# Kernel optimization log

Hardware: AMD Instinct MI355X
Metric: run time of the kernel (lower is better)

Reference implementation:

```python
import jax, jax.numpy as jnp
import numpy as np
from jax import lax
from jax.scipy.special import logsumexp

INSIZE = 256
NBASE = 4
SIZE = 2 * NBASE * (NBASE + 1)  # 40


def setup_inputs() -> dict:
    key = jax.random.key(0)
    kx, kw, kb = jax.random.split(key, 3)
    x = jax.random.normal(kx, (2048, 256, INSIZE), dtype=jnp.float32)
    W = jax.random.normal(kw, (SIZE, INSIZE), dtype=jnp.float32) / np.sqrt(INSIZE)
    b = 0.5 * jax.random.normal(kb, (SIZE,), dtype=jnp.float32)
    return {"x": x, "W": W, "b": b}


def global_norm_flipflop(scores):
    # scores: (T, N, C) with C = 2*nbase*(nbase+1)
    T, N, C = scores.shape
    nbase = int(np.sqrt(C / 2))
    assert 2 * nbase * (nbase + 1) == C

    fwd0 = jnp.zeros((N, 2 * nbase), dtype=scores.dtype)
    logZ0 = logsumexp(fwd0, axis=1, keepdims=True)  # (N, 1) = log(2*nbase)
    fwd0 = fwd0 - logZ0

    def step(carry, sc_t):
        fwd, logZ = carry
        # (N, nbase+1, 2*nbase): transition scores into each destination row
        sc = fwd[:, None, :] + sc_t.reshape(N, nbase + 1, 2 * nbase)
        base1 = logsumexp(sc[:, :nbase], axis=2)  # flip states (N, nbase)
        base2 = jnp.logaddexp(sc[:, nbase, :nbase], sc[:, nbase, nbase:])  # flop (N, nbase)
        new_state = jnp.concatenate([base1, base2], axis=1)  # (N, 2*nbase)
        factors = logsumexp(new_state, axis=1, keepdims=True)
        return (new_state - factors, logZ + factors), None

    (_, logZ), _ = lax.scan(step, (fwd0, logZ0), scores)
    return scores - logZ / T  # broadcast (N,1) over (T,N,C)


def reference(x, W, b):
    y = 5.0 * jnp.tanh(x @ W.T + b)  # (T, N, 40)
    return global_norm_flipflop(y)
```

## Files before the change

### kernel.cpp

```cpp
#include <hip/hip_runtime.h>
#include <hip/hip_bf16.h>

#define T_DIM 2048
#define N_DIM 256
#define K_DIM 256
#define C_DIM 40
#define CHUNK 32
#define NCHUNK 64
#define NTILES (T_DIM * N_DIM / 16)

#define LOG2E_F 1.44269504088896340736f
#define LN2_F   0.69314718055994530942f
#define NEGBIG  (-1.0e30f)

typedef short bf16x8 __attribute__((ext_vector_type(8)));
typedef float f32x4  __attribute__((ext_vector_type(4)));

__device__ __forceinline__ float fexp2(float x) { return exp2f(x); }
__device__ __forceinline__ float flog2(float x) { return log2f(x); }
__device__ __forceinline__ float frcp(float x) { return __frcp_rn(x); }

__device__ __forceinline__ unsigned int pk2(float a, float b)
{
    __hip_bfloat162 h = __float22bfloat162_rn(make_float2(a, b));
    unsigned int r;
    __builtin_memcpy(&r, &h, sizeof(r));
    return r;
}

__device__ __forceinline__ uint4 pack8u(float4 lo, float4 hi)
{
    uint4 t;
    t.x = pk2(lo.x, lo.y);
    t.y = pk2(lo.z, lo.w);
    t.z = pk2(hi.x, hi.y);
    t.w = pk2(hi.z, hi.w);
    return t;
}

__device__ __forceinline__ bf16x8 as_bf16x8(uint4 u)
{
    bf16x8 r;
    __builtin_memcpy(&r, &u, sizeof(r));
    return r;
}

__device__ __forceinline__ float tanh5(float v)
{
    const float e = fexp2(fabsf(v) * (2.0f * LOG2E_F));
    const float t = 1.0f - 2.0f * frcp(e + 1.0f);
    return 5.0f * copysignf(t, v);
}

__global__ __launch_bounds__(256, 4) void k1_gemm_tanh(
    const float* __restrict__ x, const float* __restrict__ W,
    const float* __restrict__ b, float* __restrict__ y)
{
    __shared__ __align__(16) uint4 wlds[24 * 64];
    __shared__ float blds[48];

    const int tid = threadIdx.x;

#pragma unroll
    for (int p = 0; p < 6; ++p) {
        const int f    = p * 256 + tid;
        const int l    = f & 63;
        const int frag = f >> 6;
        const int nt   = frag % 3;
        const int ks   = frag / 3;
        const int col  = nt * 16 + (l & 15);
        const int kg   = l >> 4;
        float4 lo = make_float4(0, 0, 0, 0), hi = lo;
        if (col < C_DIM) {
            lo = *(const float4*)(W + (size_t)col * K_DIM + ks * 32 + kg * 4);
            hi = *(const float4*)(W + (size_t)col * K_DIM + ks * 32 + 16 + kg * 4);
        }
        wlds[frag * 64 + l] = pack8u(lo, hi);
    }
    if (tid < 48) blds[tid] = (tid < C_DIM) ? b[tid] : 0.0f;
    __syncthreads();

    const int wave = tid >> 6;
    const int lane = tid & 63;
    const int lr   = lane & 15;
    const int kg   = lane >> 4;

    const float bc0 = blds[lr];
    const float bc1 = blds[16 + lr];
    const float bc2 = blds[32 + lr];

    const int wid = blockIdx.x * 4 + wave;

#pragma unroll 1
    for (int tile = wid; tile < NTILES; tile += 4096) {
        const float4* __restrict__ xp4 =
            (const float4*)(x + ((size_t)tile * 16 + lr) * K_DIM) + kg;

        f32x4 af0 = {bc0, bc0, bc0, bc0};
        f32x4 af1 = {bc1, bc1, bc1, bc1};
        f32x4 af2 = {bc2, bc2, bc2, bc2};

#pragma unroll
        for (int ks = 0; ks < 8; ++ks) {
            const float4 lo = xp4[ks * 8];
            const float4 hi = xp4[ks * 8 + 4];
            const bf16x8 a = as_bf16x8(pack8u(lo, hi));
            const bf16x8 w0 = *(const bf16x8*)&wlds[(ks * 3 + 0) * 64 + lane];
            const bf16x8 w1 = *(const bf16x8*)&wlds[(ks * 3 + 1) * 64 + lane];
            const bf16x8 w2 = *(const bf16x8*)&wlds[(ks * 3 + 2) * 64 + lane];
            af0 = __builtin_amdgcn_mfma_f32_16x16x32_bf16(a, w0, af0, 0, 0, 0);
            af1 = __builtin_amdgcn_mfma_f32_16x16x32_bf16(a, w1, af1, 0, 0, 0);
            af2 = __builtin_amdgcn_mfma_f32_16x16x32_bf16(a, w2, af2, 0, 0, 0);
        }

        float* __restrict__ yrow = y + ((size_t)tile * 16 + kg * 4) * C_DIM;
#pragma unroll
        for (int r = 0; r < 4; ++r) {
            yrow[r * C_DIM + lr]      = tanh5(af0[r]);
            yrow[r * C_DIM + 16 + lr] = tanh5(af1[r]);
            if (lr < 8)
                yrow[r * C_DIM + 32 + lr] = tanh5(af2[r]);
        }
    }
}

__global__ __launch_bounds__(256) void k2_chunks(
    const float* __restrict__ y, float* __restrict__ cmat)
{
    const int tid  = threadIdx.x;
    const int wave = tid >> 6;
    const int lane = tid & 63;
    const int task = lane >> 3;
    const int c    = lane & 7;
    const int g    = blockIdx.x & (NCHUNK - 1);
    const int n    = ((blockIdx.x >> 6) << 5) + (wave << 3) + task;

    float col[8];
#pragma unroll
    for (int j = 0; j < 8; ++j) col[j] = (j == c) ? 0.0f : NEGBIG;

    const float* __restrict__ yp =
        y + ((size_t)(g * CHUNK) * N_DIM + (size_t)n) * C_DIM;

#pragma unroll 1
    for (int s = 0; s < CHUNK; ++s) {
        float sc[C_DIM];
        const float4* p4 = (const float4*)yp;
#pragma unroll
        for (int q = 0; q < 10; ++q) {
            const float4 v = p4[q];
            sc[4 * q + 0] = v.x * LOG2E_F;
            sc[4 * q + 1] = v.y * LOG2E_F;
            sc[4 * q + 2] = v.z * LOG2E_F;
            sc[4 * q + 3] = v.w * LOG2E_F;
        }
        float nc[8];
#pragma unroll
        for (int d = 0; d < 4; ++d) {
            float tv[8];
#pragma unroll
            for (int j = 0; j < 8; ++j) tv[j] = sc[d * 8 + j] + col[j];
            float m = tv[0];
#pragma unroll
            for (int j = 1; j < 8; ++j) m = fmaxf(m, tv[j]);
            float ss = 0.0f;
#pragma unroll
            for (int j = 0; j < 8; ++j) ss += fexp2(tv[j] - m);
            nc[d] = m + flog2(ss);
        }
#pragma unroll
        for (int i = 0; i < 4; ++i) {
            const float a  = sc[32 + i] + col[i];
            const float bb = sc[36 + i] + col[i + 4];
            const float m  = fmaxf(a, bb);
            const float ss = fexp2(a - m) + fexp2(bb - m);
            nc[4 + i] = m + flog2(ss);
        }
#pragma unroll
        for (int j = 0; j < 8; ++j) col[j] = nc[j];
        yp += (size_t)N_DIM * C_DIM;
    }
    float* __restrict__ op = cmat + (((size_t)g * 8 + c) * N_DIM + n) * 8;
#pragma unroll
    for (int j = 0; j < 8; ++j) op[j] = col[j];
}

__global__ __launch_bounds__(256) void k3_combine(
    const float* __restrict__ cmat, float* __restrict__ corr)
{
    const int tid = threadIdx.x;
    const int d   = tid & 7;
    const int n   = blockIdx.x * 32 + (tid >> 3);

    float v[8];
#pragma unroll
    for (int j = 0; j < 8; ++j) v[j] = 0.0f;

#pragma unroll 1
    for (int g = 0; g < NCHUNK; ++g) {
        const float* mg = cmat + ((size_t)g * 8 * N_DIM + n) * 8 + d;
        float mm[8];
#pragma unroll
        for (int j = 0; j < 8; ++j) mm[j] = mg[(size_t)j * N_DIM * 8];
        float tv[8];
#pragma unroll
        for (int j = 0; j < 8; ++j) tv[j] = mm[j] + v[j];
        float m = tv[0];
#pragma unroll
        for (int j = 1; j < 8; ++j) m = fmaxf(m, tv[j]);
        float ss = 0.0f;
#pragma unroll
        for (int j = 0; j < 8; ++j) ss += fexp2(tv[j] - m);
        const float nv = m + flog2(ss);
#pragma unroll
        for (int j = 0; j < 8; ++j) v[j] = __shfl(nv, j, 8);
    }
    float m = v[0];
#pragma unroll
    for (int j = 1; j < 8; ++j) m = fmaxf(m, v[j]);
    float ss = 0.0f;
#pragma unroll
    for (int j = 0; j < 8; ++j) ss += fexp2(v[j] - m);
    const float lz2 = m + flog2(ss);
    if (d == 0) corr[n] = lz2 * LN2_F / (float)T_DIM;
}

__global__ __launch_bounds__(256) void k4_final(
    float* __restrict__ out, const float* __restrict__ corr)
{
    const unsigned int i = blockIdx.x * 256u + threadIdx.x;
    float4* o4 = (float4*)out;
    float4 v = o4[i];
    const unsigned int n = (i / 10u) & (N_DIM - 1);
    const float cr = corr[n];
    v.x -= cr; v.y -= cr; v.z -= cr; v.w -= cr;
    o4[i] = v;
}

extern "C" void kernel_launch(void* const* d_in, const int* in_sizes, int n_in,
                              void* d_out, int out_size, void* d_ws, size_t ws_size,
                              hipStream_t stream)
{
    const float* x = (const float*)d_in[0];
    const float* W = (const float*)d_in[1];
    const float* b = (const float*)d_in[2];
    float* y = (float*)d_out;

    float* cmat = (float*)d_ws;
    float* corr = (float*)d_ws + (size_t)NCHUNK * 8 * N_DIM * 8;

    hipLaunchKernelGGL(k1_gemm_tanh, dim3(1024), dim3(256), 0, stream, x, W, b, y);
    hipLaunchKernelGGL(k2_chunks,    dim3(512),  dim3(256), 0, stream, y, cmat);
    hipLaunchKernelGGL(k3_combine,   dim3(8),    dim3(256), 0, stream, cmat, corr);
    hipLaunchKernelGGL(k4_final,     dim3((T_DIM * N_DIM * C_DIM / 4) / 256),
                       dim3(256), 0, stream, y, corr);
}
```

Measured before the change: 264.6 us.

## Store tanh scores as bf16 intermediate and stage x through swizzled LDS with split-K waves

The GEMM kernel now loads 64-row x tiles cooperatively into XOR-swizzled shared memory as bf16. Two wave groups split K and reduce through LDS, with W fragments held in registers. The scores are written to a bf16 workspace instead of fp32 output. The recurrence and final kernels read bf16, and the final kernel writes fp32 output, which lowers intermediate traffic. This trades accuracy, since the output values are rounded to bf16, and adds block-level syncs per tile.

```diff
diff --git a/kernel.cpp b/kernel.cpp
--- a/kernel.cpp
+++ b/kernel.cpp
@@ -7,7 +7,7 @@
 #define C_DIM 40
 #define CHUNK 32
 #define NCHUNK 64
-#define NTILES (T_DIM * N_DIM / 16)
+#define NSUPER (T_DIM * N_DIM / 64)
 
 #define LOG2E_F 1.44269504088896340736f
 #define LN2_F   0.69314718055994530942f
@@ -45,6 +45,14 @@
     return r;
 }
 
+__device__ __forceinline__ unsigned short bf16r(float v)
+{
+    return (unsigned short)(pk2(v, 0.0f) & 0xffffu);
+}
+
+__device__ __forceinline__ float bl(unsigned int w) { return __uint_as_float(w << 16); }
+__device__ __forceinline__ float bh(unsigned int w) { return __uint_as_float(w & 0xffff0000u); }
+
 __device__ __forceinline__ float tanh5(float v)
 {
     const float e = fexp2(fabsf(v) * (2.0f * LOG2E_F));
@@ -52,80 +60,108 @@
     return 5.0f * copysignf(t, v);
 }
 
-__global__ __launch_bounds__(256, 4) void k1_gemm_tanh(
+__global__ __launch_bounds__(512, 4) void k1_gemm_tanh(
     const float* __restrict__ x, const float* __restrict__ W,
-    const float* __restrict__ b, float* __restrict__ y)
-{
-    __shared__ __align__(16) uint4 wlds[24 * 64];
-    __shared__ float blds[48];
-
-    const int tid = threadIdx.x;
-
-#pragma unroll
-    for (int p = 0; p < 6; ++p) {
-        const int f    = p * 256 + tid;
-        const int l    = f & 63;
-        const int frag = f >> 6;
-        const int nt   = frag % 3;
-        const int ks   = frag / 3;
-        const int col  = nt * 16 + (l & 15);
-        const int kg   = l >> 4;
-        float4 lo = make_float4(0, 0, 0, 0), hi = lo;
-        if (col < C_DIM) {
-            lo = *(const float4*)(W + (size_t)col * K_DIM + ks * 32 + kg * 4);
-            hi = *(const float4*)(W + (size_t)col * K_DIM + ks * 32 + 16 + kg * 4);
-        }
-        wlds[frag * 64 + l] = pack8u(lo, hi);
-    }
-    if (tid < 48) blds[tid] = (tid < C_DIM) ? b[tid] : 0.0f;
-    __syncthreads();
-
+    const float* __restrict__ b, unsigned short* __restrict__ yb)
+{
+    __shared__ __align__(16) unsigned char xl[64 * 512];
+    __shared__ __align__(16) float pl[4 * 12 * 64];
+
+    const int tid  = threadIdx.x;
     const int wave = tid >> 6;
     const int lane = tid & 63;
     const int lr   = lane & 15;
     const int kg   = lane >> 4;
-
-    const float bc0 = blds[lr];
-    const float bc1 = blds[16 + lr];
-    const float bc2 = blds[32 + lr];
-
-    const int wid = blockIdx.x * 4 + wave;
+    const int mt   = wave & 3;
+    const int kh   = wave >> 2;
+
+    const float bc0 = b[lr];
+    const float bc1 = b[16 + lr];
+    const float bc2 = (lr < 8) ? b[32 + lr] : 0.0f;
+
+    bf16x8 wf[4][3];
+#pragma unroll
+    for (int i = 0; i < 4; ++i) {
+        const int ks = kh * 4 + i;
+#pragma unroll
+        for (int nt = 0; nt < 3; ++nt) {
+            const int col = nt * 16 + lr;
+            float4 lo = make_float4(0, 0, 0, 0), hi = lo;
+            if (col < C_DIM) {
+                const float* wp = W + (size_t)col * K_DIM + ks * 32 + kg * 8;
+                lo = *(const float4*)wp;
+                hi = *(const float4*)(wp + 4);
+            }
+            wf[i][nt] = as_bf16x8(pack8u(lo, hi));
+        }
+    }
 
 #pragma unroll 1
-    for (int tile = wid; tile < NTILES; tile += 4096) {
-        const float4* __restrict__ xp4 =
-            (const float4*)(x + ((size_t)tile * 16 + lr) * K_DIM) + kg;
-
-        f32x4 af0 = {bc0, bc0, bc0, bc0};
-        f32x4 af1 = {bc1, bc1, bc1, bc1};
-        f32x4 af2 = {bc2, bc2, bc2, bc2};
-
-#pragma unroll
-        for (int ks = 0; ks < 8; ++ks) {
-            const float4 lo = xp4[ks * 8];
-            const float4 hi = xp4[ks * 8 + 4];
-            const bf16x8 a = as_bf16x8(pack8u(lo, hi));
-            const bf16x8 w0 = *(const bf16x8*)&wlds[(ks * 3 + 0) * 64 + lane];
-            const bf16x8 w1 = *(const bf16x8*)&wlds[(ks * 3 + 1) * 64 + lane];
-            const bf16x8 w2 = *(const bf16x8*)&wlds[(ks * 3 + 2) * 64 + lane];
-            af0 = __builtin_amdgcn_mfma_f32_16x16x32_bf16(a, w0, af0, 0, 0, 0);
-            af1 = __builtin_amdgcn_mfma_f32_16x16x32_bf16(a, w1, af1, 0, 0, 0);
-            af2 = __builtin_amdgcn_mfma_f32_16x16x32_bf16(a, w2, af2, 0, 0, 0);
-        }
-
-        float* __restrict__ yrow = y + ((size_t)tile * 16 + kg * 4) * C_DIM;
-#pragma unroll
-        for (int r = 0; r < 4; ++r) {
-            yrow[r * C_DIM + lr]      = tanh5(af0[r]);
-            yrow[r * C_DIM + 16 + lr] = tanh5(af1[r]);
-            if (lr < 8)
-                yrow[r * C_DIM + 32 + lr] = tanh5(af2[r]);
+    for (int st = blockIdx.x; st < NSUPER; st += gridDim.x) {
+        const float4* __restrict__ xg4 =
+            (const float4*)(x + (size_t)st * 64 * K_DIM);
+#pragma unroll
+        for (int p = 0; p < 8; ++p) {
+            const int f4  = p * 512 + tid;
+            const int row = f4 >> 6;
+            const int kq  = f4 & 63;
+            const float4 v = xg4[f4];
+            uint2 w2;
+            w2.x = pk2(v.x, v.y);
+            w2.y = pk2(v.z, v.w);
+            const int off = (row * 512 + kq * 8) ^ ((row & 7) << 4);
+            *(uint2*)(xl + off) = w2;
+        }
+        __syncthreads();
+
+        f32x4 af0, af1, af2;
+        if (kh == 0) {
+            af0 = (f32x4){bc0, bc0, bc0, bc0};
+            af1 = (f32x4){bc1, bc1, bc1, bc1};
+            af2 = (f32x4){bc2, bc2, bc2, bc2};
+        } else {
+            af0 = (f32x4){0.f, 0.f, 0.f, 0.f}; af1 = af0; af2 = af0;
+        }
+        const int rbase = (mt * 16 + lr) * 512;
+        const int swz   = (lr & 7) << 4;
+#pragma unroll
+        for (int i = 0; i < 4; ++i) {
+            const int ks = kh * 4 + i;
+            const bf16x8 a =
+                *(const bf16x8*)(xl + ((rbase + ks * 64 + kg * 16) ^ swz));
+            af0 = __builtin_amdgcn_mfma_f32_16x16x32_bf16(a, wf[i][0], af0, 0, 0, 0);
+            af1 = __builtin_amdgcn_mfma_f32_16x16x32_bf16(a, wf[i][1], af1, 0, 0, 0);
+            af2 = __builtin_amdgcn_mfma_f32_16x16x32_bf16(a, wf[i][2], af2, 0, 0, 0);
+        }
+
+        if (kh == 1) {
+            float* p = pl + (mt * 12) * 64 + lane;
+#pragma unroll
+            for (int j = 0; j < 4; ++j) p[j * 64]       = af0[j];
+#pragma unroll
+            for (int j = 0; j < 4; ++j) p[(4 + j) * 64] = af1[j];
+#pragma unroll
+            for (int j = 0; j < 4; ++j) p[(8 + j) * 64] = af2[j];
+        }
+        __syncthreads();
+
+        if (kh == 0) {
+            const float* p = pl + (mt * 12) * 64 + lane;
+            unsigned short* yr =
+                yb + ((size_t)st * 64 + mt * 16 + kg * 4) * C_DIM;
+#pragma unroll
+            for (int r = 0; r < 4; ++r) {
+                yr[r * C_DIM + lr]      = bf16r(tanh5(af0[r] + p[r * 64]));
+                yr[r * C_DIM + 16 + lr] = bf16r(tanh5(af1[r] + p[(4 + r) * 64]));
+                if (lr < 8)
+                    yr[r * C_DIM + 32 + lr] = bf16r(tanh5(af2[r] + p[(8 + r) * 64]));
+            }
         }
     }
 }
 
 __global__ __launch_bounds__(256) void k2_chunks(
-    const float* __restrict__ y, float* __restrict__ cmat)
+    const unsigned short* __restrict__ yb, float* __restrict__ cmat)
 {
     const int tid  = threadIdx.x;
     const int wave = tid >> 6;
@@ -139,20 +175,24 @@
 #pragma unroll
     for (int j = 0; j < 8; ++j) col[j] = (j == c) ? 0.0f : NEGBIG;
 
-    const float* __restrict__ yp =
-        y + ((size_t)(g * CHUNK) * N_DIM + (size_t)n) * C_DIM;
+    const unsigned short* __restrict__ yp =
+        yb + ((size_t)(g * CHUNK) * N_DIM + (size_t)n) * C_DIM;
 
 #pragma unroll 1
     for (int s = 0; s < CHUNK; ++s) {
         float sc[C_DIM];
-        const float4* p4 = (const float4*)yp;
-#pragma unroll
-        for (int q = 0; q < 10; ++q) {
-            const float4 v = p4[q];
-            sc[4 * q + 0] = v.x * LOG2E_F;
-            sc[4 * q + 1] = v.y * LOG2E_F;
-            sc[4 * q + 2] = v.z * LOG2E_F;
-            sc[4 * q + 3] = v.w * LOG2E_F;
+        const uint4* p4 = (const uint4*)yp;
+#pragma unroll
+        for (int q = 0; q < 5; ++q) {
+            const uint4 u = p4[q];
+            sc[8 * q + 0] = bl(u.x) * LOG2E_F;
+            sc[8 * q + 1] = bh(u.x) * LOG2E_F;
+            sc[8 * q + 2] = bl(u.y) * LOG2E_F;
+            sc[8 * q + 3] = bh(u.y) * LOG2E_F;
+            sc[8 * q + 4] = bl(u.z) * LOG2E_F;
+            sc[8 * q + 5] = bh(u.z) * LOG2E_F;
+            sc[8 * q + 6] = bl(u.w) * LOG2E_F;
+            sc[8 * q + 7] = bh(u.w) * LOG2E_F;
         }
         float nc[8];
 #pragma unroll
@@ -226,15 +266,20 @@
 }
 
 __global__ __launch_bounds__(256) void k4_final(
-    float* __restrict__ out, const float* __restrict__ corr)
-{
-    const unsigned int i = blockIdx.x * 256u + threadIdx.x;
+    const unsigned short* __restrict__ yb, const float* __restrict__ corr,
+    float* __restrict__ out)
+{
+    const int i = blockIdx.x * 256 + threadIdx.x;
+    const uint4 u = ((const uint4*)yb)[i];
+    const float cr = corr[(i / 5) & (N_DIM - 1)];
+    float4 o0, o1;
+    o0.x = bl(u.x) - cr; o0.y = bh(u.x) - cr;
+    o0.z = bl(u.y) - cr; o0.w = bh(u.y) - cr;
+    o1.x = bl(u.z) - cr; o1.y = bh(u.z) - cr;
+    o1.z = bl(u.w) - cr; o1.w = bh(u.w) - cr;
     float4* o4 = (float4*)out;
-    float4 v = o4[i];
-    const unsigned int n = (i / 10u) & (N_DIM - 1);
-    const float cr = corr[n];
-    v.x -= cr; v.y -= cr; v.z -= cr; v.w -= cr;
-    o4[i] = v;
+    o4[i * 2]     = o0;
+    o4[i * 2 + 1] = o1;
 }
 
 extern "C" void kernel_launch(void* const* d_in, const int* in_sizes, int n_in,
@@ -244,14 +289,15 @@
     const float* x = (const float*)d_in[0];
     const float* W = (const float*)d_in[1];
     const float* b = (const float*)d_in[2];
-    float* y = (float*)d_out;
-
-    float* cmat = (float*)d_ws;
-    float* corr = (float*)d_ws + (size_t)NCHUNK * 8 * N_DIM * 8;
-
-    hipLaunchKernelGGL(k1_gemm_tanh, dim3(1024), dim3(256), 0, stream, x, W, b, y);
-    hipLaunchKernelGGL(k2_chunks,    dim3(512),  dim3(256), 0, stream, y, cmat);
+    float* out = (float*)d_out;
+
+    unsigned short* ybf = (unsigned short*)d_ws;
+    float* cmat = (float*)((char*)d_ws + (48u << 20));
+    float* corr = cmat + (size_t)NCHUNK * 8 * N_DIM * 8;
+
+    hipLaunchKernelGGL(k1_gemm_tanh, dim3(1024), dim3(512), 0, stream, x, W, b, ybf);
+    hipLaunchKernelGGL(k2_chunks,    dim3(512),  dim3(256), 0, stream, ybf, cmat);
     hipLaunchKernelGGL(k3_combine,   dim3(8),    dim3(256), 0, stream, cmat, corr);
-    hipLaunchKernelGGL(k4_final,     dim3((T_DIM * N_DIM * C_DIM / 4) / 256),
-                       dim3(256), 0, stream, y, corr);
-}
+    hipLaunchKernelGGL(k4_final,     dim3(T_DIM * N_DIM * C_DIM / 8 / 256),
+                       dim3(256), 0, stream, ybf, corr, out);
+}
```

Measured after the change: 253.2 us. 1.04x faster.
